# Optimization experiments

Hardware: AMD Instinct MI355X
Metric: run time of the kernel (lower is better)

## Reference

```python
import jax, jax.numpy as jnp
import numpy as np

H = 16  # head_count
D = 1024  # model_dim
DH = D // H  # dim_per_head = 64


def setup_inputs() -> dict:
    key = jax.random.key(0)
    ks = jax.random.split(key, 16)
    B, S = 8, 1024
    inp = {
        "key": jax.random.normal(ks[0], (B, S, D), jnp.float32),
        "value": jax.random.normal(ks[1], (B, S, D), jnp.float32),
        "query": jax.random.normal(ks[2], (B, S, D), jnp.float32),
        "mask": jax.random.randint(ks[3], (B, S, S), 0, 2).astype(jnp.bool_),
        "predefined_graph_1": jax.random.uniform(ks[4], (B, S, S), jnp.float32),
        # learned params: nn.Linear(model_dim, model_dim) each, y = x @ W.T + b
        "Wq": jax.random.normal(ks[5], (D, D), jnp.float32) / np.sqrt(D),
        "bq": jnp.zeros((D,), jnp.float32),
        "Wk": jax.random.normal(ks[6], (D, D), jnp.float32) / np.sqrt(D),
        "bk": jnp.zeros((D,), jnp.float32),
        "Wv": jax.random.normal(ks[7], (D, D), jnp.float32) / np.sqrt(D),
        "bv": jnp.zeros((D,), jnp.float32),
        "Wo": jax.random.normal(ks[8], (D, D), jnp.float32) / np.sqrt(D),
        "bo": jnp.zeros((D,), jnp.float32),
    }
    return inp


def reference(key, value, query, mask, predefined_graph_1, Wq, bq, Wk, bk, Wv, bv, Wo, bo):
    B, Sq, _ = query.shape
    Sk = key.shape[1]

    def shape_heads(x, S):  # [B,S,D] -> [B,H,S,DH]
        return x.reshape(B, S, H, DH).transpose(0, 2, 1, 3)

    q = shape_heads(query @ Wq.T + bq, Sq) * (1.0 / np.sqrt(DH))
    k = shape_heads(key @ Wk.T + bk, Sk)
    v = shape_heads(value @ Wv.T + bv, Sk)

    scores = jnp.einsum("bhqd,bhkd->bhqk", q, k)  # [B,H,Sq,Sk]
    scores = jnp.where(mask[:, None, :, :], jnp.float32(-1e18), scores)
    attn = jax.nn.softmax(scores, axis=-1)

    # reweight the LAST head's attention by the predefined graph, renormalize
    am = attn[:, -1] * predefined_graph_1  # [B,Sq,Sk]
    am = am / (jnp.sum(am, axis=2, keepdims=True) + 1e-9)
    attn = jnp.concatenate([attn[:, :-1], am[:, None]], axis=1)

    # dropout p=0 (eval) -> identity
    ctx = jnp.einsum("bhqk,bhkd->bhqd", attn, v)  # [B,H,Sq,DH]
    ctx = ctx.transpose(0, 2, 1, 3).reshape(B, Sq, D)
    return ctx @ Wo.T + bo
```

## Files before the change

kernel.cpp:

```cpp
#include <hip/hip_runtime.h>
#include <hip/hip_bf16.h>

#define S_LEN 1024
#define NHEAD 16
#define MDIM  1024
#define DHEAD 64
#define BATCH 8

typedef __attribute__((ext_vector_type(8))) short bf16x8;
typedef __attribute__((ext_vector_type(4))) float f32x4;

static __device__ __forceinline__ unsigned short f2bf(float f) {
  union { float f; unsigned int u; } x; x.f = f;
  unsigned int r = x.u + 0x7fffu + ((x.u >> 16) & 1u);
  return (unsigned short)(r >> 16);
}
static __device__ __forceinline__ unsigned int pack2(float a, float b) {
  return (unsigned int)f2bf(a) | ((unsigned int)f2bf(b) << 16);
}
static __device__ __forceinline__ unsigned int cvtpk(float a, float b) {
  unsigned int r;
  asm("v_cvt_pk_bf16_f32 %0, %1, %2" : "=v"(r) : "v"(a), "v"(b));
  return r;
}
static __device__ __forceinline__ f32x4 mfma16(bf16x8 a, bf16x8 b, f32x4 c) {
  return __builtin_amdgcn_mfma_f32_16x16x32_bf16(a, b, c, 0, 0, 0);
}
static __device__ __forceinline__ bf16x8 ld_frag8(const unsigned short* p) {
  uint2 a = *(const uint2*)(p);
  uint2 b = *(const uint2*)(p + 4);
  union { uint2 u2[2]; bf16x8 v; } r; r.u2[0] = a; r.u2[1] = b;
  return r.v;
}
static __device__ __forceinline__ bf16x8 ld_frag16(const unsigned short* p) {
  union { uint4 u; bf16x8 v; } r; r.u = *(const uint4*)p;
  return r.v;
}
static __device__ __forceinline__ void gl_lds16(const unsigned short* g, unsigned short* l) {
  __builtin_amdgcn_global_load_lds(
      (const __attribute__((address_space(1))) unsigned int*)g,
      (__attribute__((address_space(3))) unsigned int*)l, 16, 0, 0);
}

__global__ __launch_bounds__(256)
void conv_w(const float* __restrict__ wq, const float* __restrict__ wk,
            const float* __restrict__ wv, const float* __restrict__ wo,
            unsigned short* __restrict__ dst)
{
  int id = blockIdx.x * 256 + threadIdx.x;
  int wi = id >> 17;
  int e  = (id & 131071) * 8;
  const float* src = (wi == 0) ? wq : (wi == 1) ? wk : (wi == 2) ? wv : wo;
  float4 f0 = *(const float4*)(src + e);
  float4 f1 = *(const float4*)(src + e + 4);
  union { unsigned int u[4]; uint4 v; } pk;
  pk.u[0] = pack2(f0.x, f0.y); pk.u[1] = pack2(f0.z, f0.w);
  pk.u[2] = pack2(f1.x, f1.y); pk.u[3] = pack2(f1.z, f1.w);
  *(uint4*)(dst + (size_t)wi * 1048576 + e) = pk.v;
}

__global__ __launch_bounds__(256)
void conv_in(const float* __restrict__ q, const float* __restrict__ k,
             const float* __restrict__ v, unsigned short* __restrict__ dst)
{
  int id = blockIdx.x * 256 + threadIdx.x;
  int wi = id >> 20;
  int e  = (id & 1048575) * 8;
  const float* src = (wi == 0) ? q : (wi == 1) ? k : v;
  float4 f0 = *(const float4*)(src + e);
  float4 f1 = *(const float4*)(src + e + 4);
  union { unsigned int u[4]; uint4 v; } pk;
  pk.u[0] = pack2(f0.x, f0.y); pk.u[1] = pack2(f0.z, f0.w);
  pk.u[2] = pack2(f1.x, f1.y); pk.u[3] = pack2(f1.z, f1.w);
  *(uint4*)(dst + (size_t)wi * 8388608 + e) = pk.v;
}

__global__ __launch_bounds__(256)
void pack_mask(const int* __restrict__ mask, unsigned long long* __restrict__ out)
{
  int i = blockIdx.x * 256 + threadIdx.x;
  unsigned long long bal = __ballot(mask[i] != 0);
  if ((threadIdx.x & 63) == 0) out[i >> 6] = bal;
}

template<bool A_BF16, bool OUT_BF16>
__device__ __forceinline__
void gemm_body(const void* __restrict__ Ap, const unsigned short* __restrict__ Wb,
               const float* __restrict__ bias, void* __restrict__ Cp, float scale)
{
  __shared__ unsigned short As[128 * 32];
  __shared__ unsigned short Bs[128 * 32];

  const int tid  = threadIdx.x;
  const int lane = tid & 63;
  const int w    = tid >> 6;
  const int lr   = lane & 15;
  const int qd   = lane >> 4;
  const int wm   = (w & 1) * 64;
  const int wn   = (w >> 1) * 64;
  const int m0   = blockIdx.x * 128;
  const int n0   = blockIdx.y * 128;

  f32x4 acc[4][4];
  #pragma unroll
  for (int i = 0; i < 4; i++)
    #pragma unroll
    for (int j = 0; j < 4; j++) acc[i][j] = {0.f, 0.f, 0.f, 0.f};

  for (int kt = 0; kt < MDIM; kt += 32) {
    #pragma unroll
    for (int it = 0; it < 2; it++) {
      int c = tid + it * 256;
      gl_lds16(Wb + (size_t)(n0 + (c >> 2)) * MDIM + kt + (c & 3) * 8, &Bs[c * 8]);
    }
    if (A_BF16) {
      #pragma unroll
      for (int it = 0; it < 2; it++) {
        int c = tid + it * 256;
        gl_lds16((const unsigned short*)Ap + (size_t)(m0 + (c >> 2)) * MDIM + kt + (c & 3) * 8,
                 &As[c * 8]);
      }
    } else {
      #pragma unroll
      for (int it = 0; it < 2; it++) {
        int c = tid + it * 256;
        int row = c >> 2, q8 = (c & 3) * 8;
        const float* src = (const float*)Ap + (size_t)(m0 + row) * MDIM + kt + q8;
        float4 f0 = *(const float4*)src;
        float4 f1 = *(const float4*)(src + 4);
        union { unsigned int u[4]; uint4 v; } pk;
        pk.u[0] = pack2(f0.x, f0.y); pk.u[1] = pack2(f0.z, f0.w);
        pk.u[2] = pack2(f1.x, f1.y); pk.u[3] = pack2(f1.z, f1.w);
        *(uint4*)&As[row * 32 + q8] = pk.v;
      }
    }
    __syncthreads();

    bf16x8 af[4], bfr[4];
    #pragma unroll
    for (int t = 0; t < 4; t++) af[t]  = ld_frag8(&As[(wm + t * 16 + lr) * 32 + qd * 8]);
    #pragma unroll
    for (int t = 0; t < 4; t++) bfr[t] = ld_frag8(&Bs[(wn + t * 16 + lr) * 32 + qd * 8]);
    #pragma unroll
    for (int i = 0; i < 4; i++)
      #pragma unroll
      for (int j = 0; j < 4; j++)
        acc[i][j] = mfma16(af[i], bfr[j], acc[i][j]);
    __syncthreads();
  }

  #pragma unroll
  for (int j = 0; j < 4; j++) {
    int n = n0 + wn + j * 16 + lr;
    float bv_ = bias[n];
    #pragma unroll
    for (int i = 0; i < 4; i++) {
      int mb = m0 + wm + i * 16 + qd * 4;
      #pragma unroll
      for (int r = 0; r < 4; r++) {
        float val = (acc[i][j][r] + bv_) * scale;
        if (OUT_BF16)
          ((unsigned short*)Cp)[(size_t)(mb + r) * MDIM + n] = f2bf(val);
        else
          ((float*)Cp)[(size_t)(mb + r) * MDIM + n] = val;
      }
    }
  }
}

template<bool A_BF16, bool OUT_BF16>
__global__ __launch_bounds__(256)
void gemm_bt(const void* __restrict__ Ap, const unsigned short* __restrict__ Wb,
             const float* __restrict__ bias, void* __restrict__ Cp, float scale)
{
  gemm_body<A_BF16, OUT_BF16>(Ap, Wb, bias, Cp, scale);
}

template<bool ABF>
__global__ __launch_bounds__(256)
void gemm_qkv(const void* __restrict__ q_in, const void* __restrict__ k_in,
              const void* __restrict__ v_in, const unsigned short* __restrict__ wbf,
              const float* __restrict__ bq, const float* __restrict__ bk,
              const float* __restrict__ bv,
              unsigned short* __restrict__ qb, unsigned short* __restrict__ kb,
              unsigned short* __restrict__ vb)
{
  const int z = blockIdx.z;
  const void* A     = (z == 0) ? q_in : (z == 1) ? k_in : v_in;
  const float* bias = (z == 0) ? bq   : (z == 1) ? bk   : bv;
  unsigned short* C = (z == 0) ? qb   : (z == 1) ? kb   : vb;
  gemm_body<ABF, true>(A, wbf + (size_t)z * 1048576, bias, C,
                       (z == 0) ? 0.125f : 1.0f);
}

#define KST 68

__global__ __launch_bounds__(256, 4)
void flash_attn(const unsigned short* __restrict__ qb,
                const unsigned short* __restrict__ kb,
                const unsigned short* __restrict__ vb,
                const unsigned long long* __restrict__ mbits,
                const float* __restrict__ graph,
                unsigned short* __restrict__ ctx)
{
  __shared__ unsigned short Ks[2][64 * 64];
  __shared__ unsigned short Vt[2][64 * KST];

  const int tid  = threadIdx.x;
  const int lane = tid & 63;
  const int w    = tid >> 6;
  const int lr   = lane & 15;
  const int qd   = lane >> 4;
  const int b    = blockIdx.x & 7;
  const int h    = blockIdx.x >> 3;
  const int qt   = blockIdx.y;
  const bool last = (h == NHEAD - 1);
  const int qrow_q = qt * 64 + w * 16 + lr;
  const int qrow0  = qt * 64 + w * 16 + qd * 4;

  const unsigned short* kb_h = kb + (size_t)b * S_LEN * MDIM + h * 64;
  const unsigned short* vb_h = vb + (size_t)b * S_LEN * MDIM + h * 64;

  const int c0 = tid, c1 = tid + 256;
  const int R0 = c0 >> 3, s0c = c0 & 7;
  const int R1 = c1 >> 3, s1c = c1 & 7;
  const int gkrow0 = 32 * (R0 >> 5) + 4 * ((R0 >> 4) & 1) + ((R0 & 12) << 1) + (R0 & 3);
  const int gkrow1 = 32 * (R1 >> 5) + 4 * ((R1 >> 4) & 1) + ((R1 & 12) << 1) + (R1 & 3);
  const int gcol0 = (s0c * 8) ^ ((R0 & 7) << 3);
  const int gcol1 = (s1c * 8) ^ ((R1 & 7) << 3);
  const unsigned short* kp0 = kb_h + (size_t)gkrow0 * MDIM + gcol0;
  const unsigned short* kp1 = kb_h + (size_t)gkrow1 * MDIM + gcol1;

  const int kswz = (lr & 7) << 4;
  const int bo0 = (((qd * 16) ^ kswz)) >> 1;
  const int bo1 = (((64 + qd * 16) ^ kswz)) >> 1;

  const unsigned short* qrowp =
      qb + ((size_t)b * S_LEN + qt * 64 + w * 16 + lr) * MDIM + h * 64;
  bf16x8 aq[2];
  #pragma unroll
  for (int ks = 0; ks < 2; ks++) aq[ks] = ld_frag16(qrowp + ks * 32 + qd * 8);

  f32x4 acc_o[4];
  #pragma unroll
  for (int g2 = 0; g2 < 4; g2++) acc_o[g2] = {0.f, 0.f, 0.f, 0.f};
  float l_main = 0.f, l_aux = 0.f;

  const int vk = (tid & 31) * 2;
  const int vd = (tid >> 5) * 8;

  const uint2* mrow = (const uint2*)mbits + (size_t)(b * S_LEN + qrow_q) * 16;
  const float* grow = graph + (size_t)(b * S_LEN + qrow_q) * S_LEN;

  gl_lds16(kp0, &Ks[0][c0 * 8]);
  gl_lds16(kp1, &Ks[0][c1 * 8]);
  {
    uint4 a = *(const uint4*)(vb_h + (size_t)vk * MDIM + vd);
    uint4 bq_ = *(const uint4*)(vb_h + (size_t)(vk + 1) * MDIM + vd);
    union { uint4 v; unsigned short s[8]; } ua, ub; ua.v = a; ub.v = bq_;
    #pragma unroll
    for (int j = 0; j < 8; j++)
      *(unsigned int*)&Vt[0][(vd + j) * KST + vk] =
          (unsigned int)ua.s[j] | ((unsigned int)ub.s[j] << 16);
  }
  __syncthreads();

  for (int t = 0; t < 16; t++) {
    const int kt2 = t * 64;
    const int cur = t & 1, nxt = (t + 1) & 1;

    uint4 pv0, pv1;
    if (t < 15) {
      gl_lds16(kp0 + (size_t)(kt2 + 64) * MDIM, &Ks[nxt][c0 * 8]);
      gl_lds16(kp1 + (size_t)(kt2 + 64) * MDIM, &Ks[nxt][c1 * 8]);
      pv0 = *(const uint4*)(vb_h + (size_t)(kt2 + 64 + vk) * MDIM + vd);
      pv1 = *(const uint4*)(vb_h + (size_t)(kt2 + 64 + vk + 1) * MDIM + vd);
    }
    uint2 mw = mrow[t];
    float4 gr4[4];
    if (last) {
      #pragma unroll
      for (int g = 0; g < 4; g++)
        gr4[g] = *(const float4*)(grow + kt2 + (g >> 1) * 32 + qd * 8 + (g & 1) * 4);
    }

    __builtin_amdgcn_s_setprio(1);
    f32x4 sc[4];
    #pragma unroll
    for (int g = 0; g < 4; g++) {
      const unsigned short* kr = &Ks[cur][(g * 16 + lr) * 64];
      f32x4 s = {0.f, 0.f, 0.f, 0.f};
      s = mfma16(ld_frag16(kr + bo0), aq[0], s);
      s = mfma16(ld_frag16(kr + bo1), aq[1], s);
      sc[g] = s;
    }
    __builtin_amdgcn_s_setprio(0);

    #pragma unroll
    for (int g = 0; g < 4; g++) {
      unsigned int wsel = (g < 2) ? mw.x : mw.y;
      #pragma unroll
      for (int r = 0; r < 4; r++) {
        bool msk = (wsel >> (qd * 8 + (g & 1) * 4 + r)) & 1u;
        float e = msk ? 0.f : __expf(sc[g][r]);
        float p = e;
        if (last) {
          l_aux += e;
          p = e * ((const float*)&gr4[g])[r];
        }
        l_main += p;
        sc[g][r] = p;
      }
    }

    union { unsigned int u[4]; bf16x8 v; } apu[2];
    #pragma unroll
    for (int g = 0; g < 4; g++)
      #pragma unroll
      for (int p = 0; p < 2; p++)
        apu[g >> 1].u[(g & 1) * 2 + p] = cvtpk(sc[g][2 * p], sc[g][2 * p + 1]);

    __builtin_amdgcn_s_setprio(1);
    #pragma unroll
    for (int g2 = 0; g2 < 4; g2++)
      #pragma unroll
      for (int ks2 = 0; ks2 < 2; ks2++)
        acc_o[g2] = mfma16(apu[ks2].v,
                           ld_frag8(&Vt[cur][(g2 * 16 + lr) * KST + ks2 * 32 + qd * 8]),
                           acc_o[g2]);
    __builtin_amdgcn_s_setprio(0);

    if (t < 15) {
      union { uint4 v; unsigned short s[8]; } ua, ub; ua.v = pv0; ub.v = pv1;
      #pragma unroll
      for (int j = 0; j < 8; j++)
        *(unsigned int*)&Vt[nxt][(vd + j) * KST + vk] =
            (unsigned int)ua.s[j] | ((unsigned int)ub.s[j] << 16);
    }
    __syncthreads();
  }

  l_main += __shfl_xor(l_main, 16, 64);
  l_main += __shfl_xor(l_main, 32, 64);
  if (last) {
    l_aux += __shfl_xor(l_aux, 16, 64);
    l_aux += __shfl_xor(l_aux, 32, 64);
  }
  float denom = last ? (l_main + 1e-9f * l_aux) : l_main;
  float inv = 1.0f / fmaxf(denom, 1e-30f);

  float inv_r[4];
  #pragma unroll
  for (int r = 0; r < 4; r++) inv_r[r] = __shfl(inv, qd * 4 + r, 64);

  #pragma unroll
  for (int g2 = 0; g2 < 4; g2++)
    #pragma unroll
    for (int r = 0; r < 4; r++)
      ctx[((size_t)b * S_LEN + qrow0 + r) * MDIM + h * 64 + g2 * 16 + lr] =
          f2bf(acc_o[g2][r] * inv_r[r]);
}

extern "C" void kernel_launch(void* const* d_in, const int* in_sizes, int n_in,
                              void* d_out, int out_size, void* d_ws, size_t ws_size,
                              hipStream_t stream) {
  const float* key_   = (const float*)d_in[0];
  const float* value_ = (const float*)d_in[1];
  const float* query_ = (const float*)d_in[2];
  const int*   mask_  = (const int*)d_in[3];
  const float* graph_ = (const float*)d_in[4];
  const float* Wq = (const float*)d_in[5];
  const float* bq = (const float*)d_in[6];
  const float* Wk = (const float*)d_in[7];
  const float* bk = (const float*)d_in[8];
  const float* Wv = (const float*)d_in[9];
  const float* bv = (const float*)d_in[10];
  const float* Wo = (const float*)d_in[11];
  const float* bo = (const float*)d_in[12];
  float* out = (float*)d_out;

  unsigned short* ws16 = (unsigned short*)d_ws;
  unsigned short* qb  = ws16;
  unsigned short* kb  = ws16 + (size_t)8 * 1024 * 1024;
  unsigned short* vb  = ws16 + (size_t)16 * 1024 * 1024;
  unsigned short* wbf = ws16 + (size_t)24 * 1024 * 1024;
  unsigned long long* mbits = (unsigned long long*)(ws16 + (size_t)28 * 1024 * 1024);
  unsigned short* qi  = ws16 + (size_t)29 * 1024 * 1024;
  unsigned short* ki  = qi + (size_t)8 * 1024 * 1024;
  unsigned short* vi  = qi + (size_t)16 * 1024 * 1024;
  const bool cvt = ws_size >= (size_t)53 * 1024 * 1024 * 2;

  dim3 bb(256, 1, 1);
  hipLaunchKernelGGL(conv_w,    dim3(2048),  bb, 0, stream, Wq, Wk, Wv, Wo, wbf);
  hipLaunchKernelGGL(pack_mask, dim3(32768), bb, 0, stream, mask_, mbits);

  dim3 gg(64, 8, 3);
  if (cvt) {
    hipLaunchKernelGGL(conv_in, dim3(12288), bb, 0, stream, query_, key_, value_, qi);
    hipLaunchKernelGGL((gemm_qkv<true>), gg, bb, 0, stream,
                       qi, ki, vi, wbf, bq, bk, bv, qb, kb, vb);
  } else {
    hipLaunchKernelGGL((gemm_qkv<false>), gg, bb, 0, stream,
                       query_, key_, value_, wbf, bq, bk, bv, qb, kb, vb);
  }
  hipLaunchKernelGGL(flash_attn, dim3(128, 16, 1), bb, 0, stream,
                     qb, kb, vb, mbits, graph_, qb );
  hipLaunchKernelGGL((gemm_bt<true, false>), dim3(64, 8), bb, 0, stream,
                     qb , wbf + 3 * 1048576, bo, out, 1.0f);
}
```

Measured before the change: 412.7 us.

## Write V transposed from projection GEMM and load it via direct LDS copies

The V projection epilogue now writes bf16 output in a per-head transposed layout [B,H,DH,S]. The attention kernel can then stage V tiles with the same async global-to-LDS path and XOR swizzle used for K. This drops the per-tile register load, 8-way scatter transpose into padded shared memory, and the extra VGPR pressure. The cost moves into the GEMM epilogue as strided 8-byte stores, which may coalesce poorly.

```diff
diff --git a/kernel.cpp b/kernel.cpp
--- a/kernel.cpp
+++ b/kernel.cpp
@@ -83,7 +83,7 @@
   if ((threadIdx.x & 63) == 0) out[i >> 6] = bal;
 }
 
-template<bool A_BF16, bool OUT_BF16>
+template<bool A_BF16, bool OUT_BF16, bool VT_OUT>
 __device__ __forceinline__
 void gemm_body(const void* __restrict__ Ap, const unsigned short* __restrict__ Wb,
                const float* __restrict__ bias, void* __restrict__ Cp, float scale)
@@ -153,16 +153,31 @@
   for (int j = 0; j < 4; j++) {
     int n = n0 + wn + j * 16 + lr;
     float bv_ = bias[n];
-    #pragma unroll
-    for (int i = 0; i < 4; i++) {
-      int mb = m0 + wm + i * 16 + qd * 4;
-      #pragma unroll
-      for (int r = 0; r < 4; r++) {
-        float val = (acc[i][j][r] + bv_) * scale;
-        if (OUT_BF16)
-          ((unsigned short*)Cp)[(size_t)(mb + r) * MDIM + n] = f2bf(val);
-        else
-          ((float*)Cp)[(size_t)(mb + r) * MDIM + n] = val;
+    if (VT_OUT) {
+      int h_ = n >> 6, d_ = n & 63;
+      #pragma unroll
+      for (int i = 0; i < 4; i++) {
+        int mb = m0 + wm + i * 16 + qd * 4;
+        int b_ = mb >> 10, s0 = mb & 1023;
+        ushort4 pk4;
+        pk4.x = f2bf(acc[i][j][0] + bv_);
+        pk4.y = f2bf(acc[i][j][1] + bv_);
+        pk4.z = f2bf(acc[i][j][2] + bv_);
+        pk4.w = f2bf(acc[i][j][3] + bv_);
+        *(ushort4*)&((unsigned short*)Cp)[(((size_t)b_ * 16 + h_) * 64 + d_) * 1024 + s0] = pk4;
+      }
+    } else {
+      #pragma unroll
+      for (int i = 0; i < 4; i++) {
+        int mb = m0 + wm + i * 16 + qd * 4;
+        #pragma unroll
+        for (int r = 0; r < 4; r++) {
+          float val = (acc[i][j][r] + bv_) * scale;
+          if (OUT_BF16)
+            ((unsigned short*)Cp)[(size_t)(mb + r) * MDIM + n] = f2bf(val);
+          else
+            ((float*)Cp)[(size_t)(mb + r) * MDIM + n] = val;
+        }
       }
     }
   }
@@ -173,7 +188,7 @@
 void gemm_bt(const void* __restrict__ Ap, const unsigned short* __restrict__ Wb,
              const float* __restrict__ bias, void* __restrict__ Cp, float scale)
 {
-  gemm_body<A_BF16, OUT_BF16>(Ap, Wb, bias, Cp, scale);
+  gemm_body<A_BF16, OUT_BF16, false>(Ap, Wb, bias, Cp, scale);
 }
 
 template<bool ABF>
@@ -183,28 +198,30 @@
               const float* __restrict__ bq, const float* __restrict__ bk,
               const float* __restrict__ bv,
               unsigned short* __restrict__ qb, unsigned short* __restrict__ kb,
-              unsigned short* __restrict__ vb)
+              unsigned short* __restrict__ vbt)
 {
   const int z = blockIdx.z;
-  const void* A     = (z == 0) ? q_in : (z == 1) ? k_in : v_in;
-  const float* bias = (z == 0) ? bq   : (z == 1) ? bk   : bv;
-  unsigned short* C = (z == 0) ? qb   : (z == 1) ? kb   : vb;
-  gemm_body<ABF, true>(A, wbf + (size_t)z * 1048576, bias, C,
-                       (z == 0) ? 0.125f : 1.0f);
-}
-
-#define KST 68
+  if (z == 2) {
+    gemm_body<ABF, true, true>(v_in, wbf + (size_t)2 * 1048576, bv, vbt, 1.0f);
+  } else {
+    const void* A     = (z == 0) ? q_in : k_in;
+    const float* bias = (z == 0) ? bq   : bk;
+    unsigned short* C = (z == 0) ? qb   : kb;
+    gemm_body<ABF, true, false>(A, wbf + (size_t)z * 1048576, bias, C,
+                                (z == 0) ? 0.125f : 1.0f);
+  }
+}
 
 __global__ __launch_bounds__(256, 4)
 void flash_attn(const unsigned short* __restrict__ qb,
                 const unsigned short* __restrict__ kb,
-                const unsigned short* __restrict__ vb,
+                const unsigned short* __restrict__ vbt,
                 const unsigned long long* __restrict__ mbits,
                 const float* __restrict__ graph,
                 unsigned short* __restrict__ ctx)
 {
   __shared__ unsigned short Ks[2][64 * 64];
-  __shared__ unsigned short Vt[2][64 * KST];
+  __shared__ unsigned short Vs[2][64 * 64];
 
   const int tid  = threadIdx.x;
   const int lane = tid & 63;
@@ -218,8 +235,8 @@
   const int qrow_q = qt * 64 + w * 16 + lr;
   const int qrow0  = qt * 64 + w * 16 + qd * 4;
 
-  const unsigned short* kb_h = kb + (size_t)b * S_LEN * MDIM + h * 64;
-  const unsigned short* vb_h = vb + (size_t)b * S_LEN * MDIM + h * 64;
+  const unsigned short* kb_h  = kb  + (size_t)b * S_LEN * MDIM + h * 64;
+  const unsigned short* vbt_h = vbt + ((size_t)b * 16 + h) * 64 * 1024;
 
   const int c0 = tid, c1 = tid + 256;
   const int R0 = c0 >> 3, s0c = c0 & 7;
@@ -230,6 +247,8 @@
   const int gcol1 = (s1c * 8) ^ ((R1 & 7) << 3);
   const unsigned short* kp0 = kb_h + (size_t)gkrow0 * MDIM + gcol0;
   const unsigned short* kp1 = kb_h + (size_t)gkrow1 * MDIM + gcol1;
+  const unsigned short* vp0 = vbt_h + (size_t)R0 * 1024 + gcol0;
+  const unsigned short* vp1 = vbt_h + (size_t)R1 * 1024 + gcol1;
 
   const int kswz = (lr & 7) << 4;
   const int bo0 = (((qd * 16) ^ kswz)) >> 1;
@@ -246,35 +265,24 @@
   for (int g2 = 0; g2 < 4; g2++) acc_o[g2] = {0.f, 0.f, 0.f, 0.f};
   float l_main = 0.f, l_aux = 0.f;
 
-  const int vk = (tid & 31) * 2;
-  const int vd = (tid >> 5) * 8;
-
   const uint2* mrow = (const uint2*)mbits + (size_t)(b * S_LEN + qrow_q) * 16;
   const float* grow = graph + (size_t)(b * S_LEN + qrow_q) * S_LEN;
 
   gl_lds16(kp0, &Ks[0][c0 * 8]);
   gl_lds16(kp1, &Ks[0][c1 * 8]);
-  {
-    uint4 a = *(const uint4*)(vb_h + (size_t)vk * MDIM + vd);
-    uint4 bq_ = *(const uint4*)(vb_h + (size_t)(vk + 1) * MDIM + vd);
-    union { uint4 v; unsigned short s[8]; } ua, ub; ua.v = a; ub.v = bq_;
-    #pragma unroll
-    for (int j = 0; j < 8; j++)
-      *(unsigned int*)&Vt[0][(vd + j) * KST + vk] =
-          (unsigned int)ua.s[j] | ((unsigned int)ub.s[j] << 16);
-  }
+  gl_lds16(vp0, &Vs[0][c0 * 8]);
+  gl_lds16(vp1, &Vs[0][c1 * 8]);
   __syncthreads();
 
   for (int t = 0; t < 16; t++) {
     const int kt2 = t * 64;
     const int cur = t & 1, nxt = (t + 1) & 1;
 
-    uint4 pv0, pv1;
     if (t < 15) {
       gl_lds16(kp0 + (size_t)(kt2 + 64) * MDIM, &Ks[nxt][c0 * 8]);
       gl_lds16(kp1 + (size_t)(kt2 + 64) * MDIM, &Ks[nxt][c1 * 8]);
-      pv0 = *(const uint4*)(vb_h + (size_t)(kt2 + 64 + vk) * MDIM + vd);
-      pv1 = *(const uint4*)(vb_h + (size_t)(kt2 + 64 + vk + 1) * MDIM + vd);
+      gl_lds16(vp0 + (kt2 + 64), &Vs[nxt][c0 * 8]);
+      gl_lds16(vp1 + (kt2 + 64), &Vs[nxt][c1 * 8]);
     }
     uint2 mw = mrow[t];
     float4 gr4[4];
@@ -322,21 +330,13 @@
 
     __builtin_amdgcn_s_setprio(1);
     #pragma unroll
-    for (int g2 = 0; g2 < 4; g2++)
-      #pragma unroll
-      for (int ks2 = 0; ks2 < 2; ks2++)
-        acc_o[g2] = mfma16(apu[ks2].v,
-                           ld_frag8(&Vt[cur][(g2 * 16 + lr) * KST + ks2 * 32 + qd * 8]),
-                           acc_o[g2]);
+    for (int g2 = 0; g2 < 4; g2++) {
+      const unsigned short* vr = &Vs[cur][(g2 * 16 + lr) * 64];
+      acc_o[g2] = mfma16(apu[0].v, ld_frag16(vr + bo0), acc_o[g2]);
+      acc_o[g2] = mfma16(apu[1].v, ld_frag16(vr + bo1), acc_o[g2]);
+    }
     __builtin_amdgcn_s_setprio(0);
 
-    if (t < 15) {
-      union { uint4 v; unsigned short s[8]; } ua, ub; ua.v = pv0; ub.v = pv1;
-      #pragma unroll
-      for (int j = 0; j < 8; j++)
-        *(unsigned int*)&Vt[nxt][(vd + j) * KST + vk] =
-            (unsigned int)ua.s[j] | ((unsigned int)ub.s[j] << 16);
-    }
     __syncthreads();
   }
 
@@ -382,7 +382,7 @@
   unsigned short* ws16 = (unsigned short*)d_ws;
   unsigned short* qb  = ws16;
   unsigned short* kb  = ws16 + (size_t)8 * 1024 * 1024;
-  unsigned short* vb  = ws16 + (size_t)16 * 1024 * 1024;
+  unsigned short* vbt = ws16 + (size_t)16 * 1024 * 1024;
   unsigned short* wbf = ws16 + (size_t)24 * 1024 * 1024;
   unsigned long long* mbits = (unsigned long long*)(ws16 + (size_t)28 * 1024 * 1024);
   unsigned short* qi  = ws16 + (size_t)29 * 1024 * 1024;
@@ -398,13 +398,13 @@
   if (cvt) {
     hipLaunchKernelGGL(conv_in, dim3(12288), bb, 0, stream, query_, key_, value_, qi);
     hipLaunchKernelGGL((gemm_qkv<true>), gg, bb, 0, stream,
-                       qi, ki, vi, wbf, bq, bk, bv, qb, kb, vb);
+                       qi, ki, vi, wbf, bq, bk, bv, qb, kb, vbt);
   } else {
     hipLaunchKernelGGL((gemm_qkv<false>), gg, bb, 0, stream,
-                       query_, key_, value_, wbf, bq, bk, bv, qb, kb, vb);
+                       query_, key_, value_, wbf, bq, bk, bv, qb, kb, vbt);
   }
   hipLaunchKernelGGL(flash_attn, dim3(128, 16, 1), bb, 0, stream,
-                     qb, kb, vb, mbits, graph_, qb );
+                     qb, kb, vbt, mbits, graph_, qb );
   hipLaunchKernelGGL((gemm_bt<true, false>), dim3(64, 8), bb, 0, stream,
                      qb , wbf + 3 * 1048576, bo, out, 1.0f);
 }
```

Measured after the change: 411.0 us. Within noise of the previous version (-0.4%).
